# Optimization experiments

Measured on AMD Instinct MI355X. Metric: run time of the kernel, lower is better.

The kernel has to match this reference:

```python
import jax, jax.numpy as jnp
import numpy as np

PI4 = np.pi / 4.0

def conv3d(x, w, b, stride):
    y = jax.lax.conv_general_dilated(
        x, w, (stride, stride, stride), ((1, 1), (1, 1), (1, 1)),
        dimension_numbers=('NCDHW', 'OIDHW', 'NCDHW'))
    return y + b[None, :, None, None, None]

def bn_relu(x, g, be):
    # BatchNorm3d in training mode: biased batch variance, eps=1e-5
    mean = jnp.mean(x, axis=(0, 2, 3, 4), keepdims=True)
    var = jnp.mean((x - mean) ** 2, axis=(0, 2, 3, 4), keepdims=True)
    xn = (x - mean) * jax.lax.rsqrt(var + 1e-5)
    return jax.nn.relu(xn * g[None, :, None, None, None] + be[None, :, None, None, None])

def _mat(b, entries):
    M = jnp.zeros((b, 4, 4), dtype=jnp.float32)
    for i, j, v in entries:
        M = M.at[:, i, j].set(v)
    return M

def affine_matrix(xs, tw, tb, rw, rb, sw, sb, shw, shb):
    b = xs.shape[0]
    one = jnp.ones((b,), xs.dtype)
    trans = jnp.tanh(xs @ tw.T + tb) * 0.1
    T = _mat(b, [(0, 0, one), (1, 1, one), (2, 2, one), (3, 3, one),
                 (0, 3, trans[:, 0]), (1, 3, trans[:, 1]), (2, 3, trans[:, 2])])
    rot = jnp.tanh(xs @ rw.T + rb) * PI4
    c, s = jnp.cos(rot), jnp.sin(rot)
    R1 = _mat(b, [(0, 0, c[:, 0]), (0, 1, -s[:, 0]), (1, 0, s[:, 0]), (1, 1, c[:, 0]), (2, 2, one), (3, 3, one)])
    R2 = _mat(b, [(1, 1, c[:, 1]), (1, 2, -s[:, 1]), (2, 1, s[:, 1]), (2, 2, c[:, 1]), (0, 0, one), (3, 3, one)])
    R3 = _mat(b, [(0, 0, c[:, 2]), (0, 1, -s[:, 2]), (1, 0, s[:, 2]), (1, 1, c[:, 2]), (2, 2, one), (3, 3, one)])
    R = R1 @ R2 @ R3
    scale = jnp.tanh(xs @ sw.T + sb) * 0.2
    e = jnp.exp(scale)
    S = _mat(b, [(0, 0, e[:, 0]), (1, 1, e[:, 1]), (2, 2, e[:, 2]), (3, 3, one)])
    sh = jnp.tanh(xs @ shw.T + shb) * PI4
    cs, ss = jnp.cos(sh), jnp.sin(sh)
    H1 = _mat(b, [(1, 1, cs[:, 0]), (1, 2, -ss[:, 0]), (2, 1, ss[:, 0]), (2, 2, cs[:, 0]), (0, 0, one), (3, 3, one)])
    H2 = _mat(b, [(0, 0, cs[:, 1]), (0, 2, ss[:, 1]), (2, 0, -ss[:, 1]), (2, 2, cs[:, 1]), (1, 1, one), (3, 3, one)])
    H3 = _mat(b, [(0, 0, cs[:, 2]), (0, 1, -ss[:, 2]), (1, 0, ss[:, 2]), (1, 1, cs[:, 2]), (2, 2, one), (3, 3, one)])
    Sh = H1 @ H2 @ H3
    # theta = Sh * S * Sh^T * R * T
    return Sh @ S @ jnp.swapaxes(Sh, 1, 2) @ R @ T

def affine_grid(theta3, size):
    b, c, D, H, W = size
    zz, yy, xx = jnp.meshgrid(jnp.linspace(-1, 1, D), jnp.linspace(-1, 1, H),
                              jnp.linspace(-1, 1, W), indexing='ij')
    mesh = jnp.stack([xx.ravel(), yy.ravel(), zz.ravel(),
                      jnp.ones(D * H * W, jnp.float32)], 0)  # (4, N)
    grid = jnp.einsum('bij,jn->bni', theta3, mesh)
    return grid.reshape(b, D, H, W, 3)

def grid_sample_3d(img, grid):
    # trilinear, align_corners=False, zero padding (matches F.grid_sample defaults)
    B, C, D, H, W = img.shape
    x = ((grid[..., 0] + 1.0) * W - 1.0) * 0.5
    y = ((grid[..., 1] + 1.0) * H - 1.0) * 0.5
    z = ((grid[..., 2] + 1.0) * D - 1.0) * 0.5
    x0, y0, z0 = jnp.floor(x), jnp.floor(y), jnp.floor(z)
    flat = img.reshape(B, C, -1)

    def corner(zc, yc, xc, w):
        valid = (zc >= 0) & (zc < D) & (yc >= 0) & (yc < H) & (xc >= 0) & (xc < W)
        zi = jnp.clip(zc, 0, D - 1).astype(jnp.int32)
        yi = jnp.clip(yc, 0, H - 1).astype(jnp.int32)
        xi = jnp.clip(xc, 0, W - 1).astype(jnp.int32)
        idx = ((zi * H + yi) * W + xi).reshape(B, 1, -1)
        v = jnp.take_along_axis(flat, jnp.broadcast_to(idx, (B, C, idx.shape[-1])), axis=2)
        return v.reshape(B, C, D, H, W) * (w * valid).reshape(B, 1, D, H, W)

    out = jnp.zeros_like(img)
    for dz in (0, 1):
        wz = (z - z0) if dz else (z0 + 1.0 - z)
        for dy in (0, 1):
            wy = (y - y0) if dy else (y0 + 1.0 - y)
            for dx in (0, 1):
                wx = (x - x0) if dx else (x0 + 1.0 - x)
                out = out + corner(z0 + dz, y0 + dy, x0 + dx, wz * wy * wx)
    return out


def setup_inputs() -> dict:
    key = jax.random.key(0)
    ks = jax.random.split(key, 10)
    B, S, nf = 16, 64, 16

    def conv_w(k, o, i):
        return jax.random.normal(k, (o, i, 3, 3, 3), jnp.float32) * (2.0 / (i * 27)) ** 0.5

    inp = {'x': jax.random.normal(ks[0], (B, 1, S, S, S), jnp.float32)}
    chans = [(1, nf), (nf, 2 * nf), (2 * nf, 4 * nf), (4 * nf, 4 * nf), (4 * nf, 4 * nf)]
    names = ['00', '0', '1', '2', '3']
    for n, (ci, co), k in zip(names, chans, ks[1:6]):
        inp['w' + n] = conv_w(k, co, ci)
        inp['b' + n] = jnp.zeros((co,), jnp.float32)
        inp['g' + n] = jnp.ones((co,), jnp.float32)
        inp['be' + n] = jnp.zeros((co,), jnp.float32)
    F = 4 * 4 * 4 * 4 * nf
    for n, k in zip(['t', 'r', 's', 'sh'], ks[6:10]):
        inp[n + 'w'] = jax.random.normal(k, (3, F), jnp.float32) * 0.01
        inp[n + 'b'] = jnp.zeros((3,), jnp.float32)
    return inp


def reference(x, w00, b00, g00, be00, w0, b0, g0, be0, w1, b1, g1, be1,
              w2, b2, g2, be2, w3, b3, g3, be3, tw, tb, rw, rb, sw, sb, shw, shb):
    xs = bn_relu(conv3d(x, w00, b00, 1), g00, be00)
    xs = bn_relu(conv3d(xs, w0, b0, 2), g0, be0)
    xs = bn_relu(conv3d(xs, w1, b1, 2), g1, be1)
    xs = bn_relu(conv3d(xs, w2, b2, 2), g2, be2)
    xs = bn_relu(conv3d(xs, w3, b3, 2), g3, be3)
    xs = xs.reshape(xs.shape[0], -1)
    theta = affine_matrix(xs, tw, tb, rw, rb, sw, sb, shw, shb)
    img = x[:, :1]
    grid = affine_grid(theta[:, :3, :], img.shape)
    return grid_sample_3d(img, grid)
```

## Files before the change

### kernel.cpp

```cpp
#include <hip/hip_runtime.h>
#include <hip/hip_bf16.h>
#include <hip/hip_fp16.h>

using bf16 = __hip_bfloat16;
static __device__ __forceinline__ float b2f(bf16 v) { return __bfloat162float(v); }

static __device__ __forceinline__ float dld(const void* p, size_t i, bool f32) {
    return f32 ? ((const float*)p)[i] : b2f(((const bf16*)p)[i]);
}

static __device__ __forceinline__ float ldf(const float* p, size_t i) { return p[i]; }
static __device__ __forceinline__ float ldf(const __half* p, size_t i) { return __half2float(p[i]); }
static __device__ __forceinline__ void stf(float* p, size_t i, float v) { p[i] = v; }
static __device__ __forceinline__ void stf(__half* p, size_t i, float v) { p[i] = __float2half(v); }

#define PI4f 0.78539816339744830961f

__global__ void detect_k(const unsigned short* __restrict__ xu,
                         float* __restrict__ flag) {
    __shared__ int sh[256];
    int tid = threadIdx.x;
    int cnt = 0;
    for (int i = tid; i < 4096; i += 256) {
        int e = (xu[i] >> 7) & 0xFF;
        if (e < 96 || e > 160) cnt++;
    }
    sh[tid] = cnt;
    __syncthreads();
    for (int off = 128; off > 0; off >>= 1) {
        if (tid < off) sh[tid] += sh[tid + off];
        __syncthreads();
    }
    if (tid == 0) flag[0] = (sh[0] > 64) ? 1.f : 0.f;
}

__global__ void zero_k(float* __restrict__ p, int n) {
    int i = threadIdx.x;
    if (i < n) p[i] = 0.f;
}

__global__ void zeroN_k(float4* __restrict__ p, int n4) {
    int i = blockIdx.x * 256 + threadIdx.x;
    if (i < n4) p[i] = make_float4(0.f, 0.f, 0.f, 0.f);
}

__global__ void wcvt_k(const void* __restrict__ w00, const void* __restrict__ w0,
                       const void* __restrict__ w1, const void* __restrict__ w2,
                       const void* __restrict__ w3, const float* __restrict__ flag,
                       float* __restrict__ dst) {
    const bool f = flag[0] != 0.f;
    int i = blockIdx.x * 256 + threadIdx.x;
    if (i < 432) {
        float v = dld(w00, i, f);
        dst[i] = v;
        int co = i / 27, tap = i % 27;
        dst[432 + tap * 16 + co] = v;
    }
    if (i < 13824) {
        float v = dld(w0, i, f);
        int co = i / 432, rem = i % 432, ci = rem / 27, tap = rem % 27;
        dst[864 + (ci * 27 + tap) * 32 + co] = v;
    }
    if (i < 55296) {
        float v = dld(w1, i, f);
        int co = i / 864, rem = i % 864, ci = rem / 27, tap = rem % 27;
        dst[14688 + (ci * 27 + tap) * 64 + co] = v;
    }
    if (i < 110592) {
        float v = dld(w2, i, f);
        int co = i / 1728, rem = i % 1728, ci = rem / 27, tap = rem % 27;
        dst[69984 + (ci * 27 + tap) * 64 + co] = v;
    }
    if (i < 110592) {
        float v = dld(w3, i, f);
        int co = i / 1728, rem = i % 1728, ci = rem / 27, tap = rem % 27;
        dst[180576 + (ci * 27 + tap) * 64 + co] = v;
    }
}

template <bool F32>
__device__ __forceinline__ void stats00_body(const void* __restrict__ xv,
                                             const float* __restrict__ wf00t,
                                             const void* __restrict__ b00,
                                             float* __restrict__ sums,
                                             float* xt, float* rs, float* rq) {
    const int tid = threadIdx.x;
    const int rbk = blockIdx.x;
    const int rx = rbk & 3, ry = (rbk >> 2) & 3, rz = rbk >> 4;
    const int b = blockIdx.z;
    const int z0 = rz * 16 - 1, y0 = ry * 16 - 1, x0 = rx * 16 - 1;
    const size_t xbase = (size_t)b * 262144;

    for (int idx = tid; idx < 5832; idx += 256) {
        int ix = idx % 18;
        int r = idx / 18;
        int iy = r % 18;
        int iz = r / 18;
        int zz = z0 + iz, yy = y0 + iy, xx = x0 + ix;
        float v = 0.f;
        if (zz >= 0 && zz < 64 && yy >= 0 && yy < 64 && xx >= 0 && xx < 64) {
            size_t gi = xbase + ((size_t)zz * 64 + yy) * 64 + xx;
            v = F32 ? ((const float*)xv)[gi] : b2f(((const bf16*)xv)[gi]);
        }
        xt[idx] = v;
    }
    if (tid < 16) { rs[tid] = 0.f; rq[tid] = 0.f; }
    __syncthreads();

    float bia[16];
#pragma unroll
    for (int c = 0; c < 16; c++) bia[c] = dld(b00, c, F32);
    float s[16], sq[16];
#pragma unroll
    for (int c = 0; c < 16; c++) { s[c] = 0.f; sq[c] = 0.f; }

    for (int k = 0; k < 16; k++) {
        int v = tid + k * 256;
        int z = v >> 8, y = (v >> 4) & 15, xw = v & 15;
        float oc[16];
#pragma unroll
        for (int c = 0; c < 16; c++) oc[c] = bia[c];
#pragma unroll
        for (int kz = 0; kz < 3; kz++)
#pragma unroll
        for (int ky = 0; ky < 3; ky++)
#pragma unroll
        for (int kx = 0; kx < 3; kx++) {
            float a = xt[(z + kz) * 324 + (y + ky) * 18 + (xw + kx)];
            const float4* w4 = (const float4*)(wf00t + ((kz * 3 + ky) * 3 + kx) * 16);
#pragma unroll
            for (int j = 0; j < 4; j++) {
                float4 wv = w4[j];
                oc[4 * j + 0] += a * wv.x;
                oc[4 * j + 1] += a * wv.y;
                oc[4 * j + 2] += a * wv.z;
                oc[4 * j + 3] += a * wv.w;
            }
        }
#pragma unroll
        for (int c = 0; c < 16; c++) { s[c] += oc[c]; sq[c] += oc[c] * oc[c]; }
    }
    const int lane = tid & 63;
#pragma unroll
    for (int c = 0; c < 16; c++) {
        float v1 = s[c], v2 = sq[c];
#pragma unroll
        for (int off = 32; off > 0; off >>= 1) {
            v1 += __shfl_down(v1, off, 64);
            v2 += __shfl_down(v2, off, 64);
        }
        if (lane == 0) { atomicAdd(&rs[c], v1); atomicAdd(&rq[c], v2); }
    }
    __syncthreads();
    if (tid < 16) {
        atomicAdd(&sums[tid], rs[tid]);
        atomicAdd(&sums[16 + tid], rq[tid]);
    }
}

__launch_bounds__(256)
__global__ void stats00_k(const void* __restrict__ x, const float* __restrict__ wf00t,
                          const void* __restrict__ b00, const float* __restrict__ flag,
                          float* __restrict__ sums) {
    __shared__ float xt[5832];
    __shared__ float rs[16], rq[16];
    if (flag[0] != 0.f) stats00_body<true>(x, wf00t, b00, sums, xt, rs, rq);
    else                stats00_body<false>(x, wf00t, b00, sums, xt, rs, rq);
}

template <bool F32, typename TOUT>
__device__ __forceinline__ void conv0f_body(
    const void* __restrict__ xv, const float* __restrict__ wf00,
    const void* __restrict__ b00, const float* __restrict__ wf0t,
    const void* __restrict__ b0v, const void* __restrict__ g00,
    const void* __restrict__ be00, const float* __restrict__ sums00,
    TOUT* __restrict__ y0, float* xt, float* yt) {
    constexpr int YTXP = 18;
    constexpr int YROW = 17 * YTXP;
    constexpr int YTOT = 9 * 17 * 17;
    constexpr int XTY = 19, XTX = 19, XTOT = 11 * 19 * 19;

    const int tid = threadIdx.x;
    const int tbk = blockIdx.x;
    const int tx = tbk & 3;
    const int ty = (tbk >> 2) & 3;
    const int tz = tbk >> 4;
    const int b = blockIdx.z;

    const int ox = tid & 7, oy = (tid >> 3) & 7, oz = tid >> 6;
    const int gz = tz * 4 + oz, gy = ty * 8 + oy, gx = tx * 8 + ox;

    const int iz0 = tz * 8 - 1, iy0 = ty * 16 - 1, ix0 = tx * 16 - 1;
    const int xz0 = iz0 - 1, xy0 = iy0 - 1, xx0 = ix0 - 1;

    const size_t xbase = (size_t)b * 262144;
    for (int idx = tid; idx < XTOT; idx += 256) {
        int ix = idx % XTX;
        int r = idx / XTX;
        int iy = r % XTY;
        int iz = r / XTY;
        int zz = xz0 + iz, yy = xy0 + iy, xx = xx0 + ix;
        float v = 0.f;
        if (zz >= 0 && zz < 64 && yy >= 0 && yy < 64 && xx >= 0 && xx < 64) {
            size_t gi = xbase + ((size_t)zz * 64 + yy) * 64 + xx;
            v = F32 ? ((const float*)xv)[gi] : b2f(((const bf16*)xv)[gi]);
        }
        xt[idx] = v;
    }

    float acc[32];
#pragma unroll
    for (int i = 0; i < 32; i++) acc[i] = 0.f;

    for (int ci = 0; ci < 16; ci++) {
        float mean = sums00[ci] * (1.f / 4194304.f);
        float var = sums00[16 + ci] * (1.f / 4194304.f) - mean * mean;
        float A = dld(g00, ci, F32) * rsqrtf(var + 1e-5f);
        float Bs = dld(be00, ci, F32) - mean * A;
        const float* wrp = wf00 + ci * 27;
        const float bia = dld(b00, ci, F32);
        __syncthreads();
        for (int idx = tid; idx < YTOT; idx += 256) {
            int ix = idx % 17;
            int r = idx / 17;
            int iy = r % 17;
            int iz = r / 17;
            int zz = iz0 + iz, yy = iy0 + iy, xx = ix0 + ix;
            float v = 0.f;
            if (zz >= 0 && zz < 64 && yy >= 0 && yy < 64 && xx >= 0 && xx < 64) {
                float o = bia;
#pragma unroll
                for (int kz = 0; kz < 3; kz++)
#pragma unroll
                for (int ky = 0; ky < 3; ky++)
#pragma unroll
                for (int kx = 0; kx < 3; kx++)
                    o += xt[(iz + kz) * (XTY * XTX) + (iy + ky) * XTX + (ix + kx)] *
                         wrp[(kz * 3 + ky) * 3 + kx];
                v = fmaxf(0.f, A * o + Bs);
            }
            yt[iz * YROW + iy * YTXP + ((ix >> 1) + (ix & 1) * 9)] = v;
        }
        __syncthreads();
#pragma unroll
        for (int kz = 0; kz < 3; kz++)
#pragma unroll
        for (int ky = 0; ky < 3; ky++)
#pragma unroll
        for (int kx = 0; kx < 3; kx++) {
            const int xcol = (kx & 1) ? (9 + ox) : (ox + (kx >> 1));
            float a = yt[(oz * 2 + kz) * YROW + (oy * 2 + ky) * YTXP + xcol];
            const int tap = (kz * 3 + ky) * 3 + kx;
            const float4* wp4 = (const float4*)(wf0t + (ci * 27 + tap) * 32);
#pragma unroll
            for (int j = 0; j < 8; j++) {
                float4 wv = wp4[j];
                acc[4 * j + 0] += a * wv.x;
                acc[4 * j + 1] += a * wv.y;
                acc[4 * j + 2] += a * wv.z;
                acc[4 * j + 3] += a * wv.w;
            }
        }
    }
    const size_t outSp = 32768;
    const size_t obase = ((size_t)b * 32) * outSp + ((size_t)gz * 32 + gy) * 32 + gx;
#pragma unroll
    for (int co = 0; co < 32; co++)
        stf(y0, obase + (size_t)co * outSp, acc[co] + dld(b0v, co, F32));
}

template <typename TOUT>
__launch_bounds__(256)
__global__ void conv0f_k(const void* __restrict__ x, const float* __restrict__ wf00,
                         const void* __restrict__ b00, const float* __restrict__ wf0t,
                         const void* __restrict__ b0v, const void* __restrict__ g00,
                         const void* __restrict__ be00,
                         const float* __restrict__ sums00,
                         const float* __restrict__ flag, TOUT* __restrict__ y0) {
    __shared__ float xt[11 * 19 * 19];
    __shared__ float yt[9 * 17 * 18];
    if (flag[0] != 0.f)
        conv0f_body<true>(x, wf00, b00, wf0t, b0v, g00, be00, sums00, y0, xt, yt);
    else
        conv0f_body<false>(x, wf00, b00, wf0t, b0v, g00, be00, sums00, y0, xt, yt);
}

template <typename TIN, int CIN, int COUT, int COACC, int NCHUNK, int TZ, int TY,
          int TX, int STRIDE, int IND, int OUTD>
__launch_bounds__(TZ * TY * TX)
__global__ void convsplit_k(const TIN* __restrict__ inv,
                            const float* __restrict__ wft,
                            const void* __restrict__ bias,
                            const void* __restrict__ g_prev,
                            const void* __restrict__ be_prev,
                            const float* __restrict__ stats_prev,
                            float Ninv_prev, const float* __restrict__ flag,
                            float* __restrict__ out) {
    static_assert(STRIDE == 2, "even/odd tile layout assumes stride 2");
    constexpr int NT = TZ * TY * TX;
    constexpr int ITZ = (TZ - 1) * STRIDE + 3;
    constexpr int ITY = (TY - 1) * STRIDE + 3;
    constexpr int ITX = (TX - 1) * STRIDE + 3;
    constexpr int ITXP = ITX + 1;
    constexpr int HALF = (ITX + 1) / 2;
    constexpr int ITOT = ITZ * ITY * ITX;
    constexpr int NTX = OUTD / TX, NTY = OUTD / TY;
    constexpr int CICH = CIN / NCHUNK;
    constexpr int NCO = COUT / COACC;

    __shared__ float tile[ITZ * ITY * ITXP];

    const bool F = flag[0] != 0.f;
    const int tid = threadIdx.x;
    const int tbk = blockIdx.x;
    const int tx = tbk % NTX;
    const int t2 = tbk / NTX;
    const int ty = t2 % NTY;
    const int tz = t2 / NTY;
    const int coBase = (blockIdx.y % NCO) * COACC;
    const int chunk = blockIdx.y / NCO;
    const int b = blockIdx.z;

    const int ox = tid % TX;
    const int oy = (tid / TX) % TY;
    const int oz = tid / (TX * TY);
    const int gz = tz * TZ + oz, gy = ty * TY + oy, gx = tx * TX + ox;

    float acc[COACC];
#pragma unroll
    for (int i = 0; i < COACC; i++) acc[i] = 0.f;

    const int iz0 = tz * TZ * STRIDE - 1;
    const int iy0 = ty * TY * STRIDE - 1;
    const int ix0 = tx * TX * STRIDE - 1;

    for (int ci = chunk * CICH; ci < (chunk + 1) * CICH; ci++) {
        float mean = stats_prev[ci] * Ninv_prev;
        float var = stats_prev[CIN + ci] * Ninv_prev - mean * mean;
        float A = dld(g_prev, ci, F) * rsqrtf(var + 1e-5f);
        float Bs = dld(be_prev, ci, F) - mean * A;
        __syncthreads();
        const size_t chanBase = ((size_t)(b * CIN + ci)) * IND * IND * IND;
        for (int idx = tid; idx < ITOT; idx += NT) {
            int ix = idx % ITX;
            int r = idx / ITX;
            int iy = r % ITY;
            int iz = r / ITY;
            int zz = iz0 + iz, yy = iy0 + iy, xx = ix0 + ix;
            float v = 0.f;
            if (zz >= 0 && zz < IND && yy >= 0 && yy < IND && xx >= 0 && xx < IND) {
                float raw = ldf(inv, chanBase + ((size_t)zz * IND + yy) * IND + xx);
                v = fmaxf(0.f, A * raw + Bs);
            }
            tile[(iz * ITY + iy) * ITXP + ((ix >> 1) + (ix & 1) * HALF)] = v;
        }
        __syncthreads();
#pragma unroll
        for (int kz = 0; kz < 3; kz++)
#pragma unroll
        for (int ky = 0; ky < 3; ky++)
#pragma unroll
        for (int kx = 0; kx < 3; kx++) {
            const int xcol = (kx & 1) ? (HALF + ox) : (ox + (kx >> 1));
            float a = tile[((oz * STRIDE + kz) * ITY + (oy * STRIDE + ky)) * ITXP +
                           xcol];
            const int tap = (kz * 3 + ky) * 3 + kx;
            const float4* wp4 =
                (const float4*)(wft + (size_t)(ci * 27 + tap) * COUT + coBase);
#pragma unroll
            for (int j = 0; j < COACC / 4; j++) {
                float4 wv = wp4[j];
                acc[4 * j + 0] += a * wv.x;
                acc[4 * j + 1] += a * wv.y;
                acc[4 * j + 2] += a * wv.z;
                acc[4 * j + 3] += a * wv.w;
            }
        }
    }
    const size_t outSp = (size_t)OUTD * OUTD * OUTD;
    const size_t obase = ((size_t)b * COUT + coBase) * outSp +
                         ((size_t)gz * OUTD + gy) * OUTD + gx;
#pragma unroll
    for (int co = 0; co < COACC; co++) {
        float v = acc[co];
        if (chunk == 0) v += dld(bias, coBase + co, F);
        atomicAdd(&out[obase + (size_t)co * outSp], v);
    }
}

template <typename T>
__global__ void stats_k(const T* __restrict__ raw, float* __restrict__ sums,
                        int C, int spatial, int B) {
    const int c = blockIdx.x;
    const int K = gridDim.y;
    const int part = blockIdx.y;
    float s = 0.f, sq = 0.f;
    for (int b = 0; b < B; b++) {
        const T* p = raw + ((size_t)(b * C + c)) * spatial;
        if constexpr (sizeof(T) == 4) {
            const float4* p4 = (const float4*)p;
            for (int i = part * blockDim.x + threadIdx.x; i < (spatial >> 2);
                 i += K * blockDim.x) {
                float4 v = p4[i];
                s += v.x + v.y + v.z + v.w;
                sq += v.x * v.x + v.y * v.y + v.z * v.z + v.w * v.w;
            }
        } else {
            for (int i = part * blockDim.x + threadIdx.x; i < spatial;
                 i += K * blockDim.x) {
                float v = ldf(p, i);
                s += v;
                sq += v * v;
            }
        }
    }
    __shared__ float rs[256], rq[256];
    int tid = threadIdx.x;
    rs[tid] = s;
    rq[tid] = sq;
    __syncthreads();
    for (int off = blockDim.x / 2; off > 0; off >>= 1) {
        if (tid < off) { rs[tid] += rs[tid + off]; rq[tid] += rq[tid + off]; }
        __syncthreads();
    }
    if (tid == 0) {
        atomicAdd(&sums[c], rs[0]);
        atomicAdd(&sums[C + c], rq[0]);
    }
}

static __device__ __forceinline__ void mm4(const float* A, const float* B, float* C) {
    for (int i = 0; i < 4; i++)
        for (int j = 0; j < 4; j++) {
            float s = 0.f;
            for (int k = 0; k < 4; k++) s += A[i * 4 + k] * B[k * 4 + j];
            C[i * 4 + j] = s;
        }
}
static __device__ __forceinline__ void ident(float* M) {
    for (int i = 0; i < 16; i++) M[i] = (i % 5 == 0) ? 1.f : 0.f;
}

__global__ void fc_affine_k(const float* __restrict__ y3,
                            const float* __restrict__ stats3,
                            const void* __restrict__ g3, const void* __restrict__ be3,
                            const void* __restrict__ tw, const void* __restrict__ tbv,
                            const void* __restrict__ rw, const void* __restrict__ rbv,
                            const void* __restrict__ sw, const void* __restrict__ sbv,
                            const void* __restrict__ shw, const void* __restrict__ shbv,
                            const float* __restrict__ flag,
                            float* __restrict__ theta) {
    const bool F = flag[0] != 0.f;
    const int b = blockIdx.x;
    const int tid = threadIdx.x;
    __shared__ float Ab[64], Bb[64];
    if (tid < 64) {
        float mean = stats3[tid] * (1.f / 1024.f);
        float var = stats3[64 + tid] * (1.f / 1024.f) - mean * mean;
        float A = dld(g3, tid, F) * rsqrtf(var + 1e-5f);
        Ab[tid] = A;
        Bb[tid] = dld(be3, tid, F) - mean * A;
    }
    __syncthreads();
    float acc[12];
#pragma unroll
    for (int j = 0; j < 12; j++) acc[j] = 0.f;
    const float* yb = y3 + (size_t)b * 4096;
    for (int f = tid; f < 4096; f += 256) {
        int c = f >> 6;
        float x = fmaxf(0.f, Ab[c] * yb[f] + Bb[c]);
#pragma unroll
        for (int i = 0; i < 3; i++) {
            acc[0 + i] += x * dld(tw, i * 4096 + f, F);
            acc[3 + i] += x * dld(rw, i * 4096 + f, F);
            acc[6 + i] += x * dld(sw, i * 4096 + f, F);
            acc[9 + i] += x * dld(shw, i * 4096 + f, F);
        }
    }
    __shared__ float red[256];
    __shared__ float dots[12];
    for (int j = 0; j < 12; j++) {
        red[tid] = acc[j];
        __syncthreads();
        for (int off = 128; off > 0; off >>= 1) {
            if (tid < off) red[tid] += red[tid + off];
            __syncthreads();
        }
        if (tid == 0) dots[j] = red[0];
        __syncthreads();
    }
    if (tid == 0) {
        float trans[3], rot[3], scl[3], sh[3];
        for (int i = 0; i < 3; i++) {
            trans[i] = 0.1f * tanhf(dots[0 + i] + dld(tbv, i, F));
            rot[i]   = PI4f * tanhf(dots[3 + i] + dld(rbv, i, F));
            scl[i]   = 0.2f * tanhf(dots[6 + i] + dld(sbv, i, F));
            sh[i]    = PI4f * tanhf(dots[9 + i] + dld(shbv, i, F));
        }
        float T[16], R1[16], R2[16], R3[16], S[16], H1[16], H2[16], H3[16];
        float t1[16], t2[16], R[16], Sh[16], ShT[16], M[16];
        ident(T); T[3] = trans[0]; T[7] = trans[1]; T[11] = trans[2];
        { float c = cosf(rot[0]), s = sinf(rot[0]);
          ident(R1); R1[0] = c; R1[1] = -s; R1[4] = s; R1[5] = c; }
        { float c = cosf(rot[1]), s = sinf(rot[1]);
          ident(R2); R2[5] = c; R2[6] = -s; R2[9] = s; R2[10] = c; }
        { float c = cosf(rot[2]), s = sinf(rot[2]);
          ident(R3); R3[0] = c; R3[1] = -s; R3[4] = s; R3[5] = c; }
        mm4(R1, R2, t1); mm4(t1, R3, R);
        ident(S); S[0] = expf(scl[0]); S[5] = expf(scl[1]); S[10] = expf(scl[2]);
        { float c = cosf(sh[0]), s = sinf(sh[0]);
          ident(H1); H1[5] = c; H1[6] = -s; H1[9] = s; H1[10] = c; }
        { float c = cosf(sh[1]), s = sinf(sh[1]);
          ident(H2); H2[0] = c; H2[2] = s; H2[8] = -s; H2[10] = c; }
        { float c = cosf(sh[2]), s = sinf(sh[2]);
          ident(H3); H3[0] = c; H3[1] = -s; H3[4] = s; H3[5] = c; }
        mm4(H1, H2, t1); mm4(t1, H3, Sh);
        for (int i = 0; i < 4; i++)
            for (int j = 0; j < 4; j++) ShT[i * 4 + j] = Sh[j * 4 + i];
        mm4(Sh, S, t1); mm4(t1, ShT, t2); mm4(t2, R, t1); mm4(t1, T, M);
        for (int i = 0; i < 12; i++) theta[b * 12 + i] = M[i];
    }
}

template <bool F32>
__device__ __forceinline__ void sample_body(const void* __restrict__ xv,
                                            const float* __restrict__ theta,
                                            void* __restrict__ out) {
    const int b = blockIdx.y;
    const int v = blockIdx.x * 256 + threadIdx.x;
    const int w = v & 63, h = (v >> 6) & 63, d = v >> 12;
    const float* t = theta + b * 12;
    const float px = -1.f + w * (2.f / 63.f);
    const float py = -1.f + h * (2.f / 63.f);
    const float pz = -1.f + d * (2.f / 63.f);
    const float gx = t[0] * px + t[1] * py + t[2] * pz + t[3];
    const float gy = t[4] * px + t[5] * py + t[6] * pz + t[7];
    const float gz = t[8] * px + t[9] * py + t[10] * pz + t[11];
    const float fx = ((gx + 1.f) * 64.f - 1.f) * 0.5f;
    const float fy = ((gy + 1.f) * 64.f - 1.f) * 0.5f;
    const float fz = ((gz + 1.f) * 64.f - 1.f) * 0.5f;
    const float x0 = floorf(fx), y0 = floorf(fy), z0 = floorf(fz);
    const float wx1 = fx - x0, wy1 = fy - y0, wz1 = fz - z0;
    const size_t ibase = (size_t)b * 262144;
    float outv = 0.f;
#pragma unroll
    for (int dz = 0; dz < 2; dz++) {
        float wz = dz ? wz1 : 1.f - wz1;
        int zc = (int)z0 + dz;
        bool zok = (zc >= 0 && zc < 64);
        int zi = min(max(zc, 0), 63);
#pragma unroll
        for (int dy = 0; dy < 2; dy++) {
            float wy = dy ? wy1 : 1.f - wy1;
            int yc = (int)y0 + dy;
            bool yok = (yc >= 0 && yc < 64);
            int yi = min(max(yc, 0), 63);
#pragma unroll
            for (int dx = 0; dx < 2; dx++) {
                float wwx = dx ? wx1 : 1.f - wx1;
                int xc = (int)x0 + dx;
                bool xok = (xc >= 0 && xc < 64);
                int xi = min(max(xc, 0), 63);
                size_t gi = ibase + ((size_t)zi * 64 + yi) * 64 + xi;
                float val = F32 ? ((const float*)xv)[gi] : b2f(((const bf16*)xv)[gi]);
                float wgt = (zok && yok && xok) ? wz * wy * wwx : 0.f;
                outv += val * wgt;
            }
        }
    }
    const size_t oi = (size_t)b * 262144 + v;
    if (F32) ((float*)out)[oi] = outv;
    else ((bf16*)out)[oi] = __float2bfloat16(outv);
}

__global__ void sample_k(const void* __restrict__ x, const float* __restrict__ theta,
                         const float* __restrict__ flag, void* __restrict__ out) {
    if (flag[0] != 0.f) sample_body<true>(x, theta, out);
    else                sample_body<false>(x, theta, out);
}

extern "C" void kernel_launch(void* const* d_in, const int* in_sizes, int n_in,
                              void* d_out, int out_size, void* d_ws, size_t ws_size,
                              hipStream_t stream) {
    const void* x    = d_in[0];
    const void* w00  = d_in[1];
    const void* b00  = d_in[2];
    const void* g00  = d_in[3];
    const void* be00 = d_in[4];
    const void* w0   = d_in[5];
    const void* b0   = d_in[6];
    const void* g0   = d_in[7];
    const void* be0  = d_in[8];
    const void* w1   = d_in[9];
    const void* b1   = d_in[10];
    const void* g1   = d_in[11];
    const void* be1  = d_in[12];
    const void* w2   = d_in[13];
    const void* b2   = d_in[14];
    const void* g2   = d_in[15];
    const void* be2  = d_in[16];
    const void* w3   = d_in[17];
    const void* b3   = d_in[18];
    const void* g3   = d_in[19];
    const void* be3  = d_in[20];
    const void* tw   = d_in[21];
    const void* tb   = d_in[22];
    const void* rw   = d_in[23];
    const void* rb   = d_in[24];
    const void* sw   = d_in[25];
    const void* sb   = d_in[26];
    const void* shw  = d_in[27];
    const void* shb  = d_in[28];

    float* wsF = (float*)d_ws;
    const bool f32path = ws_size >= (size_t)21853232 * 4;
    const size_t Y0U = f32path ? 16777216 : 8388608;
    const size_t Y1_OFF = Y0U;
    const size_t Y2_OFF = Y1_OFF + 4194304;
    const size_t Y3_OFF = Y2_OFF + 524288;
    const size_t WF_OFF = Y3_OFF + 65536;
    const size_t ST_OFF = WF_OFF + 291200;
    const size_t FL_OFF = ST_OFF + 480;
    const size_t TH_OFF = ST_OFF + 496;

    float* y1 = wsF + Y1_OFF;
    float* y2 = wsF + Y2_OFF;
    float* y3 = wsF + Y3_OFF;
    float* wf00  = wsF + WF_OFF + 0;
    float* wf00t = wsF + WF_OFF + 432;
    float* wf0t  = wsF + WF_OFF + 864;
    float* wf1t  = wsF + WF_OFF + 14688;
    float* wf2t  = wsF + WF_OFF + 69984;
    float* wf3t  = wsF + WF_OFF + 180576;
    float* sums00 = wsF + ST_OFF + 0;
    float* sums0  = wsF + ST_OFF + 32;
    float* sums1  = wsF + ST_OFF + 96;
    float* sums2  = wsF + ST_OFF + 224;
    float* sums3  = wsF + ST_OFF + 352;
    float* flag   = wsF + FL_OFF;
    float* theta  = wsF + TH_OFF;

    zero_k<<<1, 512, 0, stream>>>(wsF + ST_OFF, 480);
    zeroN_k<<<4672, 256, 0, stream>>>((float4*)y1, 1196032);
    detect_k<<<1, 256, 0, stream>>>((const unsigned short*)x, flag);
    wcvt_k<<<432, 256, 0, stream>>>(w00, w0, w1, w2, w3, flag, wsF + WF_OFF);

    stats00_k<<<dim3(64, 1, 16), 256, 0, stream>>>(x, wf00t, b00, flag, sums00);

    if (f32path) {
        float* y0 = wsF;
        conv0f_k<float><<<dim3(128, 1, 16), 256, 0, stream>>>(
            x, wf00, b00, wf0t, b0, g00, be00, sums00, flag, y0);
        stats_k<float><<<dim3(32, 32), 256, 0, stream>>>(y0, sums0, 32, 32768, 16);
        convsplit_k<float, 32, 64, 32, 2, 4, 8, 8, 2, 32, 16>
            <<<dim3(16, 4, 16), 256, 0, stream>>>(y0, wf1t, b1, g0, be0, sums0,
                                                  1.f / 524288.f, flag, y1);
    } else {
        __half* y0 = (__half*)d_ws;
        conv0f_k<__half><<<dim3(128, 1, 16), 256, 0, stream>>>(
            x, wf00, b00, wf0t, b0, g00, be00, sums00, flag, y0);
        stats_k<__half><<<dim3(32, 32), 256, 0, stream>>>(y0, sums0, 32, 32768, 16);
        convsplit_k<__half, 32, 64, 32, 2, 4, 8, 8, 2, 32, 16>
            <<<dim3(16, 4, 16), 256, 0, stream>>>(y0, wf1t, b1, g0, be0, sums0,
                                                  1.f / 524288.f, flag, y1);
    }

    stats_k<float><<<dim3(64, 4), 256, 0, stream>>>(y1, sums1, 64, 4096, 16);

    convsplit_k<float, 64, 64, 16, 8, 2, 8, 8, 2, 16, 8>
        <<<dim3(4, 32, 16), 128, 0, stream>>>(y1, wf2t, b2, g1, be1, sums1,
                                              1.f / 65536.f, flag, y2);
    stats_k<float><<<dim3(64, 1), 256, 0, stream>>>(y2, sums2, 64, 512, 16);

    convsplit_k<float, 64, 64, 16, 16, 4, 4, 4, 2, 8, 4>
        <<<dim3(1, 64, 16), 64, 0, stream>>>(y2, wf3t, b3, g2, be2, sums2,
                                             1.f / 8192.f, flag, y3);
    stats_k<float><<<dim3(64, 1), 256, 0, stream>>>(y3, sums3, 64, 64, 16);

    fc_affine_k<<<16, 256, 0, stream>>>(y3, sums3, g3, be3, tw, tb, rw, rb, sw, sb,
                                        shw, shb, flag, theta);

    sample_k<<<dim3(1024, 16), 256, 0, stream>>>(x, theta, flag, d_out);
}
```

Before: 979.6 us.

## Process four input channels per pass in fused conv00+conv0 with float4 swizzled tile

```diff
diff --git a/kernel.cpp b/kernel.cpp
--- a/kernel.cpp
+++ b/kernel.cpp
@@ -169,16 +169,14 @@
 }
 
 template <bool F32, typename TOUT>
-__device__ __forceinline__ void conv0f_body(
-    const void* __restrict__ xv, const float* __restrict__ wf00,
+__device__ __forceinline__ void conv0g_body(
+    const void* __restrict__ xv, const float* __restrict__ wf00t,
     const void* __restrict__ b00, const float* __restrict__ wf0t,
     const void* __restrict__ b0v, const void* __restrict__ g00,
     const void* __restrict__ be00, const float* __restrict__ sums00,
-    TOUT* __restrict__ y0, float* xt, float* yt) {
-    constexpr int YTXP = 18;
-    constexpr int YROW = 17 * YTXP;
-    constexpr int YTOT = 9 * 17 * 17;
+    TOUT* __restrict__ y0, float* __restrict__ xt, float4* __restrict__ yt) {
     constexpr int XTY = 19, XTX = 19, XTOT = 11 * 19 * 19;
+    constexpr int RS = 25;
 
     const int tid = threadIdx.x;
     const int tbk = blockIdx.x;
@@ -212,34 +210,49 @@
 #pragma unroll
     for (int i = 0; i < 32; i++) acc[i] = 0.f;
 
-    for (int ci = 0; ci < 16; ci++) {
-        float mean = sums00[ci] * (1.f / 4194304.f);
-        float var = sums00[16 + ci] * (1.f / 4194304.f) - mean * mean;
-        float A = dld(g00, ci, F32) * rsqrtf(var + 1e-5f);
-        float Bs = dld(be00, ci, F32) - mean * A;
-        const float* wrp = wf00 + ci * 27;
-        const float bia = dld(b00, ci, F32);
+    for (int g = 0; g < 4; g++) {
+        float A[4], Bs[4], bia[4];
+#pragma unroll
+        for (int j = 0; j < 4; j++) {
+            const int ci = g * 4 + j;
+            float mean = sums00[ci] * (1.f / 4194304.f);
+            float var = sums00[16 + ci] * (1.f / 4194304.f) - mean * mean;
+            A[j] = dld(g00, ci, F32) * rsqrtf(var + 1e-5f);
+            Bs[j] = dld(be00, ci, F32) - mean * A[j];
+            bia[j] = dld(b00, ci, F32);
+        }
         __syncthreads();
-        for (int idx = tid; idx < YTOT; idx += 256) {
-            int ix = idx % 17;
+        for (int idx = tid; idx < 2601; idx += 256) {
+            int ixp = idx % 17;
             int r = idx / 17;
-            int iy = r % 17;
-            int iz = r / 17;
-            int zz = iz0 + iz, yy = iy0 + iy, xx = ix0 + ix;
-            float v = 0.f;
+            int iyp = r % 17;
+            int izp = r / 17;
+            int zz = iz0 + izp, yy = iy0 + iyp, xx = ix0 + ixp;
+            float4 v = make_float4(0.f, 0.f, 0.f, 0.f);
             if (zz >= 0 && zz < 64 && yy >= 0 && yy < 64 && xx >= 0 && xx < 64) {
-                float o = bia;
+                float o0 = bia[0], o1 = bia[1], o2 = bia[2], o3 = bia[3];
 #pragma unroll
                 for (int kz = 0; kz < 3; kz++)
 #pragma unroll
                 for (int ky = 0; ky < 3; ky++)
 #pragma unroll
-                for (int kx = 0; kx < 3; kx++)
-                    o += xt[(iz + kz) * (XTY * XTX) + (iy + ky) * XTX + (ix + kx)] *
-                         wrp[(kz * 3 + ky) * 3 + kx];
-                v = fmaxf(0.f, A * o + Bs);
+                for (int kx = 0; kx < 3; kx++) {
+                    float a = xt[(izp + kz) * (XTY * XTX) + (iyp + ky) * XTX +
+                                 (ixp + kx)];
+                    float4 wv = *(const float4*)(wf00t +
+                                                 ((kz * 3 + ky) * 3 + kx) * 16 +
+                                                 g * 4);
+                    o0 += a * wv.x;
+                    o1 += a * wv.y;
+                    o2 += a * wv.z;
+                    o3 += a * wv.w;
+                }
+                v.x = fmaxf(0.f, A[0] * o0 + Bs[0]);
+                v.y = fmaxf(0.f, A[1] * o1 + Bs[1]);
+                v.z = fmaxf(0.f, A[2] * o2 + Bs[2]);
+                v.w = fmaxf(0.f, A[3] * o3 + Bs[3]);
             }
-            yt[iz * YROW + iy * YTXP + ((ix >> 1) + (ix & 1) * 9)] = v;
+            yt[(izp * 17 + iyp) * RS + (ixp ^ ((iyp >> 1) & 7))] = v;
         }
         __syncthreads();
 #pragma unroll
@@ -248,17 +261,23 @@
         for (int ky = 0; ky < 3; ky++)
 #pragma unroll
         for (int kx = 0; kx < 3; kx++) {
-            const int xcol = (kx & 1) ? (9 + ox) : (ox + (kx >> 1));
-            float a = yt[(oz * 2 + kz) * YROW + (oy * 2 + ky) * YTXP + xcol];
+            const int riy = oy * 2 + ky;
+            const int row = (oz * 2 + kz) * 17 + riy;
+            float4 a4 = yt[row * RS + ((ox * 2 + kx) ^ ((riy >> 1) & 7))];
             const int tap = (kz * 3 + ky) * 3 + kx;
-            const float4* wp4 = (const float4*)(wf0t + (ci * 27 + tap) * 32);
-#pragma unroll
-            for (int j = 0; j < 8; j++) {
-                float4 wv = wp4[j];
-                acc[4 * j + 0] += a * wv.x;
-                acc[4 * j + 1] += a * wv.y;
-                acc[4 * j + 2] += a * wv.z;
-                acc[4 * j + 3] += a * wv.w;
+            const float* wbase = wf0t + (size_t)(g * 4 * 27 + tap) * 32;
+#pragma unroll
+            for (int j = 0; j < 4; j++) {
+                float aj = (j == 0) ? a4.x : (j == 1) ? a4.y : (j == 2) ? a4.z : a4.w;
+                const float4* wp4 = (const float4*)(wbase + (size_t)j * 27 * 32);
+#pragma unroll
+                for (int q = 0; q < 8; q++) {
+                    float4 wv = wp4[q];
+                    acc[4 * q + 0] += aj * wv.x;
+                    acc[4 * q + 1] += aj * wv.y;
+                    acc[4 * q + 2] += aj * wv.z;
+                    acc[4 * q + 3] += aj * wv.w;
+                }
             }
         }
     }
@@ -271,18 +290,18 @@
 
 template <typename TOUT>
 __launch_bounds__(256)
-__global__ void conv0f_k(const void* __restrict__ x, const float* __restrict__ wf00,
+__global__ void conv0g_k(const void* __restrict__ x, const float* __restrict__ wf00t,
                          const void* __restrict__ b00, const float* __restrict__ wf0t,
                          const void* __restrict__ b0v, const void* __restrict__ g00,
                          const void* __restrict__ be00,
                          const float* __restrict__ sums00,
                          const float* __restrict__ flag, TOUT* __restrict__ y0) {
     __shared__ float xt[11 * 19 * 19];
-    __shared__ float yt[9 * 17 * 18];
+    __shared__ float4 yt[9 * 17 * 25];
     if (flag[0] != 0.f)
-        conv0f_body<true>(x, wf00, b00, wf0t, b0v, g00, be00, sums00, y0, xt, yt);
+        conv0g_body<true>(x, wf00t, b00, wf0t, b0v, g00, be00, sums00, y0, xt, yt);
     else
-        conv0f_body<false>(x, wf00, b00, wf0t, b0v, g00, be00, sums00, y0, xt, yt);
+        conv0g_body<false>(x, wf00t, b00, wf0t, b0v, g00, be00, sums00, y0, xt, yt);
 }
 
 template <typename TIN, int CIN, int COUT, int COACC, int NCHUNK, int TZ, int TY,
@@ -383,8 +402,12 @@
 #pragma unroll
     for (int co = 0; co < COACC; co++) {
         float v = acc[co];
-        if (chunk == 0) v += dld(bias, coBase + co, F);
-        atomicAdd(&out[obase + (size_t)co * outSp], v);
+        if constexpr (NCHUNK == 1) {
+            out[obase + (size_t)co * outSp] = v + dld(bias, coBase + co, F);
+        } else {
+            if (chunk == 0) v += dld(bias, coBase + co, F);
+            atomicAdd(&out[obase + (size_t)co * outSp], v);
+        }
     }
 }
 
@@ -649,16 +672,16 @@
 
     if (f32path) {
         float* y0 = wsF;
-        conv0f_k<float><<<dim3(128, 1, 16), 256, 0, stream>>>(
-            x, wf00, b00, wf0t, b0, g00, be00, sums00, flag, y0);
+        conv0g_k<float><<<dim3(128, 1, 16), 256, 0, stream>>>(
+            x, wf00t, b00, wf0t, b0, g00, be00, sums00, flag, y0);
         stats_k<float><<<dim3(32, 32), 256, 0, stream>>>(y0, sums0, 32, 32768, 16);
         convsplit_k<float, 32, 64, 32, 2, 4, 8, 8, 2, 32, 16>
             <<<dim3(16, 4, 16), 256, 0, stream>>>(y0, wf1t, b1, g0, be0, sums0,
                                                   1.f / 524288.f, flag, y1);
     } else {
         __half* y0 = (__half*)d_ws;
-        conv0f_k<__half><<<dim3(128, 1, 16), 256, 0, stream>>>(
-            x, wf00, b00, wf0t, b0, g00, be00, sums00, flag, y0);
+        conv0g_k<__half><<<dim3(128, 1, 16), 256, 0, stream>>>(
+            x, wf00t, b00, wf0t, b0, g00, be00, sums00, flag, y0);
         stats_k<__half><<<dim3(32, 32), 256, 0, stream>>>(y0, sums0, 32, 32768, 16);
         convsplit_k<__half, 32, 64, 32, 2, 4, 8, 8, 2, 32, 16>
             <<<dim3(16, 4, 16), 256, 0, stream>>>(y0, wf1t, b1, g0, be0, sums0,
```

Result: slower. 1.204 ms (+22.9%).

## Materialize first conv output in halves and run second conv via generic split kernel

Applied to the files above, without the earlier changes.

```diff
diff --git a/kernel.cpp b/kernel.cpp
--- a/kernel.cpp
+++ b/kernel.cpp
@@ -78,18 +78,20 @@
     }
 }
 
-template <bool F32>
+template <bool F32, bool DOSTATS, bool STORE>
 __device__ __forceinline__ void stats00_body(const void* __restrict__ xv,
                                              const float* __restrict__ wf00t,
                                              const void* __restrict__ b00,
                                              float* __restrict__ sums,
+                                             float* __restrict__ y00, int batchOff,
                                              float* xt, float* rs, float* rq) {
     const int tid = threadIdx.x;
     const int rbk = blockIdx.x;
     const int rx = rbk & 3, ry = (rbk >> 2) & 3, rz = rbk >> 4;
-    const int b = blockIdx.z;
+    const int zb = blockIdx.z;
+    const int rb = zb + batchOff;
     const int z0 = rz * 16 - 1, y0 = ry * 16 - 1, x0 = rx * 16 - 1;
-    const size_t xbase = (size_t)b * 262144;
+    const size_t xbase = (size_t)rb * 262144;
 
     for (int idx = tid; idx < 5832; idx += 256) {
         int ix = idx % 18;
@@ -104,7 +106,7 @@
         }
         xt[idx] = v;
     }
-    if (tid < 16) { rs[tid] = 0.f; rq[tid] = 0.f; }
+    if (DOSTATS && tid < 16) { rs[tid] = 0.f; rq[tid] = 0.f; }
     __syncthreads();
 
     float bia[16];
@@ -137,35 +139,52 @@
                 oc[4 * j + 3] += a * wv.w;
             }
         }
-#pragma unroll
-        for (int c = 0; c < 16; c++) { s[c] += oc[c]; sq[c] += oc[c] * oc[c]; }
-    }
-    const int lane = tid & 63;
-#pragma unroll
-    for (int c = 0; c < 16; c++) {
-        float v1 = s[c], v2 = sq[c];
-#pragma unroll
-        for (int off = 32; off > 0; off >>= 1) {
-            v1 += __shfl_down(v1, off, 64);
-            v2 += __shfl_down(v2, off, 64);
-        }
-        if (lane == 0) { atomicAdd(&rs[c], v1); atomicAdd(&rq[c], v2); }
-    }
-    __syncthreads();
-    if (tid < 16) {
-        atomicAdd(&sums[tid], rs[tid]);
-        atomicAdd(&sums[16 + tid], rq[tid]);
-    }
-}
-
+        if constexpr (STORE) {
+            const size_t sp = (((size_t)(rz * 16 + z) * 64 + (ry * 16 + y)) * 64) +
+                              (rx * 16 + xw);
+#pragma unroll
+            for (int c = 0; c < 16; c++)
+                y00[(((size_t)(zb * 16 + c)) << 18) + sp] = oc[c];
+        }
+        if constexpr (DOSTATS) {
+#pragma unroll
+            for (int c = 0; c < 16; c++) { s[c] += oc[c]; sq[c] += oc[c] * oc[c]; }
+        }
+    }
+    if constexpr (DOSTATS) {
+        const int lane = tid & 63;
+#pragma unroll
+        for (int c = 0; c < 16; c++) {
+            float v1 = s[c], v2 = sq[c];
+#pragma unroll
+            for (int off = 32; off > 0; off >>= 1) {
+                v1 += __shfl_down(v1, off, 64);
+                v2 += __shfl_down(v2, off, 64);
+            }
+            if (lane == 0) { atomicAdd(&rs[c], v1); atomicAdd(&rq[c], v2); }
+        }
+        __syncthreads();
+        if (tid < 16) {
+            atomicAdd(&sums[tid], rs[tid]);
+            atomicAdd(&sums[16 + tid], rq[tid]);
+        }
+    }
+}
+
+template <bool DOSTATS, bool STORE>
 __launch_bounds__(256)
 __global__ void stats00_k(const void* __restrict__ x, const float* __restrict__ wf00t,
                           const void* __restrict__ b00, const float* __restrict__ flag,
-                          float* __restrict__ sums) {
+                          float* __restrict__ sums, float* __restrict__ y00,
+                          int batchOff) {
     __shared__ float xt[5832];
     __shared__ float rs[16], rq[16];
-    if (flag[0] != 0.f) stats00_body<true>(x, wf00t, b00, sums, xt, rs, rq);
-    else                stats00_body<false>(x, wf00t, b00, sums, xt, rs, rq);
+    if (flag[0] != 0.f)
+        stats00_body<true, DOSTATS, STORE>(x, wf00t, b00, sums, y00, batchOff,
+                                           xt, rs, rq);
+    else
+        stats00_body<false, DOSTATS, STORE>(x, wf00t, b00, sums, y00, batchOff,
+                                            xt, rs, rq);
 }
 
 template <bool F32, typename TOUT>
@@ -383,8 +402,12 @@
 #pragma unroll
     for (int co = 0; co < COACC; co++) {
         float v = acc[co];
-        if (chunk == 0) v += dld(bias, coBase + co, F);
-        atomicAdd(&out[obase + (size_t)co * outSp], v);
+        if constexpr (NCHUNK == 1) {
+            out[obase + (size_t)co * outSp] = v + dld(bias, coBase + co, F);
+        } else {
+            if (chunk == 0) v += dld(bias, coBase + co, F);
+            atomicAdd(&out[obase + (size_t)co * outSp], v);
+        }
     }
 }
 
@@ -614,6 +637,7 @@
 
     float* wsF = (float*)d_ws;
     const bool f32path = ws_size >= (size_t)21853232 * 4;
+    const bool mat = ws_size >= (size_t)(21853232 + 33554432) * 4;
     const size_t Y0U = f32path ? 16777216 : 8388608;
     const size_t Y1_OFF = Y0U;
     const size_t Y2_OFF = Y1_OFF + 4194304;
@@ -639,16 +663,36 @@
     float* sums3  = wsF + ST_OFF + 352;
     float* flag   = wsF + FL_OFF;
     float* theta  = wsF + TH_OFF;
+    float* y00f   = wsF + 21853232;
 
     zero_k<<<1, 512, 0, stream>>>(wsF + ST_OFF, 480);
     zeroN_k<<<4672, 256, 0, stream>>>((float4*)y1, 1196032);
     detect_k<<<1, 256, 0, stream>>>((const unsigned short*)x, flag);
     wcvt_k<<<432, 256, 0, stream>>>(w00, w0, w1, w2, w3, flag, wsF + WF_OFF);
 
-    stats00_k<<<dim3(64, 1, 16), 256, 0, stream>>>(x, wf00t, b00, flag, sums00);
-
-    if (f32path) {
+    if (f32path && mat) {
         float* y0 = wsF;
+        stats00_k<true, true><<<dim3(64, 1, 8), 256, 0, stream>>>(
+            x, wf00t, b00, flag, sums00, y00f, 0);
+        stats00_k<true, false><<<dim3(64, 1, 8), 256, 0, stream>>>(
+            x, wf00t, b00, flag, sums00, nullptr, 8);
+        convsplit_k<float, 16, 32, 32, 1, 4, 8, 8, 2, 64, 32>
+            <<<dim3(128, 1, 8), 256, 0, stream>>>(y00f, wf0t, b0, g00, be00,
+                                                  sums00, 1.f / 4194304.f, flag, y0);
+        stats00_k<false, true><<<dim3(64, 1, 8), 256, 0, stream>>>(
+            x, wf00t, b00, flag, sums00, y00f, 8);
+        convsplit_k<float, 16, 32, 32, 1, 4, 8, 8, 2, 64, 32>
+            <<<dim3(128, 1, 8), 256, 0, stream>>>(y00f, wf0t, b0, g00, be00,
+                                                  sums00, 1.f / 4194304.f, flag,
+                                                  y0 + (size_t)8 * 32 * 32768);
+        stats_k<float><<<dim3(32, 32), 256, 0, stream>>>(y0, sums0, 32, 32768, 16);
+        convsplit_k<float, 32, 64, 32, 2, 4, 8, 8, 2, 32, 16>
+            <<<dim3(16, 4, 16), 256, 0, stream>>>(y0, wf1t, b1, g0, be0, sums0,
+                                                  1.f / 524288.f, flag, y1);
+    } else if (f32path) {
+        float* y0 = wsF;
+        stats00_k<true, false><<<dim3(64, 1, 16), 256, 0, stream>>>(
+            x, wf00t, b00, flag, sums00, nullptr, 0);
         conv0f_k<float><<<dim3(128, 1, 16), 256, 0, stream>>>(
             x, wf00, b00, wf0t, b0, g00, be00, sums00, flag, y0);
         stats_k<float><<<dim3(32, 32), 256, 0, stream>>>(y0, sums0, 32, 32768, 16);
@@ -657,6 +701,8 @@
                                                   1.f / 524288.f, flag, y1);
     } else {
         __half* y0 = (__half*)d_ws;
+        stats00_k<true, false><<<dim3(64, 1, 16), 256, 0, stream>>>(
+            x, wf00t, b00, flag, sums00, nullptr, 0);
         conv0f_k<__half><<<dim3(128, 1, 16), 256, 0, stream>>>(
             x, wf00, b00, wf0t, b0, g00, be00, sums00, flag, y0);
         stats_k<__half><<<dim3(32, 32), 256, 0, stream>>>(y0, sums0, 32, 32768, 16);
```

Result: slower. 1.148 ms (+17.2%).
